# Kernel optimization log

Measured on AMD Instinct MI355X. Metric: run time of the kernel, lower is better.

The kernel has to match this reference:

```python
import jax, jax.numpy as jnp
import numpy as np

# Model dims (match init_kwargs)
E = 2048   # embed_dim
H = 16     # num_heads
QR = 512   # q_low_rank
KVR = 512  # kv_low_rank
DR = 64    # rope_dim
DV = 128   # v_head_dim
S = 2048   # seq_len


def _make_rotary(seq_len, dim):
    inv_freq = 1.0 / jnp.power(10000.0, jnp.arange(0, dim, 2, dtype=jnp.float32) / dim)
    t = jnp.arange(seq_len, dtype=jnp.float32)
    freqs = jnp.outer(t, inv_freq)  # (S, dim//2)
    return jnp.sin(freqs), jnp.cos(freqs)


def _apply_rope(x, sin, cos):
    # x: (S, H_or_1, D); sin/cos: (S, D//2)
    d = x.shape[-1] // 2
    x1, x2 = x[..., :d], x[..., d:]
    s = jnp.concatenate([sin, sin], axis=-1)[:, None, :]
    c = jnp.concatenate([cos, cos], axis=-1)[:, None, :]
    return x * c + jnp.concatenate([-x2, x1], axis=-1) * s


def setup_inputs() -> dict:
    key = jax.random.key(0)
    ks = jax.random.split(key, 8)
    def lin(k, out_dim, in_dim):
        return jax.random.normal(k, (out_dim, in_dim), dtype=jnp.float32) * (1.0 / np.sqrt(in_dim))
    return {
        "x": jax.random.normal(ks[0], (S, E), dtype=jnp.float32),
        "wq_down": lin(ks[1], QR, E),
        "wq_up": lin(ks[2], H * DV, QR),
        "wq_rope": lin(ks[3], H * DR, QR),
        "wkv_down": lin(ks[4], KVR, E),
        "wkv_up": lin(ks[5], H * 2 * DV, KVR),
        "wk_rope": lin(ks[6], DR, E),
        "wo": lin(ks[7], E, H * DV),
    }


def reference(x, wq_down, wq_up, wq_rope, wkv_down, wkv_up, wk_rope, wo):
    seq = x.shape[0]
    # Query path: low-rank bottleneck -> content + rope streams
    c_q = x @ wq_down.T                                   # (S, QR)
    q_content = (c_q @ wq_up.T).reshape(seq, H, DV)       # (S, H, DV)
    q_rope = (c_q @ wq_rope.T).reshape(seq, H, DR)        # (S, H, DR)
    # KV path: shared low-rank bottleneck
    c_kv = x @ wkv_down.T                                 # (S, KVR)
    kv = c_kv @ wkv_up.T                                  # (S, 2*H*DV)
    k_content_flat, v_flat = jnp.split(kv, 2, axis=-1)
    k_content = k_content_flat.reshape(seq, H, DV)
    v = v_flat.reshape(seq, H, DV)
    # Shared key-RoPE projection (one per position, broadcast over heads)
    k_rope_shared = (x @ wk_rope.T)[:, None, :]           # (S, 1, DR)
    sin, cos = _make_rotary(seq, DR)
    q_rope_rot = _apply_rope(q_rope, sin, cos)            # (S, H, DR)
    k_rope_rot = _apply_rope(k_rope_shared, sin, cos)     # (S, 1, DR)
    # Concat content + rope streams; QK head dim = DV + DR
    dt = jnp.bfloat16
    q = jnp.concatenate([q_content, q_rope_rot], axis=-1).astype(dt)                            # (S, H, DV+DR)
    k = jnp.concatenate([k_content, jnp.broadcast_to(k_rope_rot, (seq, H, DR))], axis=-1).astype(dt)
    v_attn = v.astype(dt)
    scale = 1.0 / np.sqrt(DV + DR)
    # Attention. Note: original zero-pads V to DV+DR then slices output back to
    # DV -- mathematically identical to attending with unpadded V.
    logits = jnp.einsum('shd,thd->hst', q, k).astype(jnp.float32) * scale  # (H, S, S)
    probs = jax.nn.softmax(logits, axis=-1).astype(dt)
    attn = jnp.einsum('hst,thd->shd', probs, v_attn)      # (S, H, DV)
    attn_flat = attn.reshape(seq, H * DV)
    return (attn_flat @ wo.T).astype(jnp.float32)         # (S, E)
```

## Files before the change

kernel.cpp:

```cpp
#include <hip/hip_runtime.h>
#include <stdint.h>
#include <math.h>

#define S_LEN 2048
#define NH 16

typedef __attribute__((ext_vector_type(8))) short bf16x8;
typedef __attribute__((ext_vector_type(4))) float f32x4;
typedef __attribute__((ext_vector_type(16))) float f32x16;
typedef unsigned short ush;

__device__ __forceinline__ ush f2bf(float f) {
  union { float f; unsigned u; } v; v.f = f;
  unsigned x = v.u;
  return (ush)((x + 0x7fffu + ((x >> 16) & 1u)) >> 16);
}
__device__ __forceinline__ float bf2f(ush b) {
  union { unsigned u; float f; } v; v.u = ((unsigned)b) << 16;
  return v.f;
}
__device__ __forceinline__ ush f2h(float f) {
  _Float16 h = (_Float16)f;
  union { _Float16 h; ush u; } v; v.h = h;
  return v.u;
}
__device__ __forceinline__ float h2f(ush u) {
  union { ush u; _Float16 h; } v; v.u = u;
  return (float)v.h;
}
__device__ __forceinline__ uint2 sx32(uint2 v) {
  uint2 r;
  r.x = (unsigned)__shfl_xor((int)v.x, 32, 64);
  r.y = (unsigned)__shfl_xor((int)v.y, 32, 64);
  return r;
}

__device__ __forceinline__ void gload_lds16(const ush* g, ush* l) {
  __builtin_amdgcn_global_load_lds((const __attribute__((address_space(1))) void*)g,
                                   (__attribute__((address_space(3))) void*)l, 16, 0, 0);
}

__global__ void mega_pack(const float* __restrict__ wq_down, const float* __restrict__ wkv_down,
                          const float* __restrict__ wk_rope, const float* __restrict__ wq_up,
                          const float* __restrict__ wq_rope, const float* __restrict__ wkv_up,
                          const float* __restrict__ wo, const float* __restrict__ x,
                          ush* __restrict__ wdh, ush* __restrict__ wqh, ush* __restrict__ wkvuh,
                          ush* __restrict__ woh, ush* __restrict__ xh, float* __restrict__ tab) {
  int idx = blockIdx.x * 256 + threadIdx.x;
  if (idx < 2359296) {
    int r = idx >> 11, c = idx & 2047;
    float v = (r < 512) ? wq_down[(size_t)r * 2048 + c]
            : (r < 1024) ? wkv_down[(size_t)(r - 512) * 2048 + c]
            : (r < 1088) ? wk_rope[(size_t)(r - 1024) * 2048 + c] : 0.f;
    wdh[idx] = f2h(v);
    return;
  }
  idx -= 2359296;
  if (idx < 1572864) {
    int r = idx >> 9, c = idx & 511;
    float v = (r < 2048) ? wq_up[(size_t)r * 512 + c] : wq_rope[(size_t)(r - 2048) * 512 + c];
    wqh[idx] = f2h(v);
    return;
  }
  idx -= 1572864;
  if (idx < 2097152) { wkvuh[idx] = f2h(wkv_up[idx]); return; }
  idx -= 2097152;
  if (idx < 4194304) { woh[idx] = f2h(wo[idx]); return; }
  idx -= 4194304;
  if (idx < 4194304) { xh[idx] = f2h(x[idx]); return; }
  idx -= 4194304;
  if (idx < 65536) {
    int tt = idx >> 5, i = idx & 31;
    float inv_freq = 1.0f / powf(10000.0f, (float)i * (1.0f / 32.0f));
    float fr = (float)tt * inv_freq;
    tab[idx] = sinf(fr);
    tab[65536 + idx] = cosf(fr);
  }
}

__global__ __launch_bounds__(256) void gemm_down(
    const ush* __restrict__ A, const ush* __restrict__ B,
    ush* __restrict__ cqh, ush* __restrict__ ckvh, float* __restrict__ krl) {
  constexpr int K = 2048;
  __shared__ __align__(16) ush As[64 * 32];
  __shared__ __align__(16) ush Bs[64 * 32];
  const int t = threadIdx.x, l = t & 63, w = t >> 6;
  const int wm = w & 1, wn = w >> 1;
  const int m0 = blockIdx.y * 64, n0 = blockIdx.x * 64;
  const int lm = l & 15, lq = l >> 4;
  const int lr = l >> 2, lc = (l & 3) * 8;

  f32x4 acc[2][2];
  const f32x4 zero = {0.f, 0.f, 0.f, 0.f};
#pragma unroll
  for (int i = 0; i < 2; i++)
#pragma unroll
    for (int j = 0; j < 2; j++) acc[i][j] = zero;

  const ush* Ag = A + (size_t)(m0 + w * 16 + lr) * K + lc;
  const ush* Bg = B + (size_t)(n0 + w * 16 + lr) * K + lc;
  ush* Al = As + w * 512;
  ush* Bl = Bs + w * 512;

  for (int k0 = 0; k0 < K; k0 += 32) {
    __syncthreads();
    gload_lds16(Ag + k0, Al);
    gload_lds16(Bg + k0, Bl);
    __syncthreads();
    bf16x8 af[2], bfr[2];
#pragma unroll
    for (int i = 0; i < 2; i++)
      af[i] = *(const bf16x8*)(As + (wm * 32 + i * 16 + lm) * 32 + lq * 8);
#pragma unroll
    for (int j = 0; j < 2; j++)
      bfr[j] = *(const bf16x8*)(Bs + (wn * 32 + j * 16 + lm) * 32 + lq * 8);
#pragma unroll
    for (int i = 0; i < 2; i++)
#pragma unroll
      for (int j = 0; j < 2; j++)
        acc[i][j] = __builtin_amdgcn_mfma_f32_16x16x32_f16(af[i], bfr[j], acc[i][j], 0, 0, 0);
  }

#pragma unroll
  for (int i = 0; i < 2; i++)
#pragma unroll
    for (int j = 0; j < 2; j++)
#pragma unroll
      for (int r = 0; r < 4; r++) {
        int mm = m0 + wm * 32 + i * 16 + lq * 4 + r;
        int nn = n0 + wn * 32 + j * 16 + lm;
        float v = acc[i][j][r];
        if (nn < 512)       cqh[(size_t)mm * 512 + nn] = f2h(v);
        else if (nn < 1024) ckvh[(size_t)mm * 512 + nn - 512] = f2h(v);
        else if (nn < 1088) krl[(size_t)mm * 64 + nn - 1024] = v;
      }
}

__global__ __launch_bounds__(256) void gemm_up(
    const ush* __restrict__ cqh, const ush* __restrict__ wqh,
    const ush* __restrict__ ckvh, const ush* __restrict__ wkvuh,
    ush* __restrict__ qupf, ush* __restrict__ kvf) {
  constexpr int BM = 128, BN = 64, K = 512, FI = 4, FJ = 2;
  __shared__ __align__(16) ush As[BM * 32];
  __shared__ __align__(16) ush Bs[BN * 32];
  int bx = blockIdx.x;
  const ush* A; const ush* B; ush* C; int ldc;
  if (bx < 48) { A = cqh; B = wqh; C = qupf; ldc = 3072; }
  else { bx -= 48; A = ckvh; B = wkvuh; C = kvf; ldc = 4096; }
  const int t = threadIdx.x, l = t & 63, w = t >> 6;
  const int wm = w & 1, wn = w >> 1;
  const int m0 = blockIdx.y * BM, n0 = bx * BN;
  const int lm = l & 15, lq = l >> 4;
  const int lr = l >> 2, lc = (l & 3) * 8;

  f32x4 acc[FI][FJ];
  const f32x4 zero = {0.f, 0.f, 0.f, 0.f};
#pragma unroll
  for (int i = 0; i < FI; i++)
#pragma unroll
    for (int j = 0; j < FJ; j++) acc[i][j] = zero;

  const ush* Ag[2];
#pragma unroll
  for (int i = 0; i < 2; i++) Ag[i] = A + (size_t)(m0 + w * 32 + i * 16 + lr) * K + lc;
  const ush* Bg = B + (size_t)(n0 + w * 16 + lr) * K + lc;
  ush* Al = As + w * (BM * 8);
  ush* Bl = Bs + w * (BN * 8);

  for (int k0 = 0; k0 < K; k0 += 32) {
    __syncthreads();
#pragma unroll
    for (int i = 0; i < 2; i++) gload_lds16(Ag[i] + k0, Al + i * 512);
    gload_lds16(Bg + k0, Bl);
    __syncthreads();
    bf16x8 af[FI], bfr[FJ];
#pragma unroll
    for (int i = 0; i < FI; i++)
      af[i] = *(const bf16x8*)(As + (wm * 64 + i * 16 + lm) * 32 + lq * 8);
#pragma unroll
    for (int j = 0; j < FJ; j++)
      bfr[j] = *(const bf16x8*)(Bs + (wn * 32 + j * 16 + lm) * 32 + lq * 8);
#pragma unroll
    for (int i = 0; i < FI; i++)
#pragma unroll
      for (int j = 0; j < FJ; j++)
        acc[i][j] = __builtin_amdgcn_mfma_f32_16x16x32_f16(af[i], bfr[j], acc[i][j], 0, 0, 0);
  }

#pragma unroll
  for (int i = 0; i < FI; i++)
#pragma unroll
    for (int j = 0; j < FJ; j++)
#pragma unroll
      for (int r = 0; r < 4; r++) {
        int mm = m0 + wm * 64 + i * 16 + lq * 4 + r;
        int nn = n0 + wn * 32 + j * 16 + lm;
        C[(size_t)mm * ldc + nn] = f2h(acc[i][j][r]);
      }
}

__global__ __launch_bounds__(256) void gemm_out(
    const ush* __restrict__ A, const ush* __restrict__ B, float* __restrict__ C,
    int K, int ldc) {
  constexpr int BM = 128, BN = 64, FI = 4, FJ = 2;
  __shared__ __align__(16) ush As[BM * 32];
  __shared__ __align__(16) ush Bs[BN * 32];
  const int t = threadIdx.x, l = t & 63, w = t >> 6;
  const int wm = w & 1, wn = w >> 1;
  const int m0 = blockIdx.y * BM, n0 = blockIdx.x * BN;
  const int lm = l & 15, lq = l >> 4;
  const int lr = l >> 2, lc = (l & 3) * 8;

  f32x4 acc[FI][FJ];
  const f32x4 zero = {0.f, 0.f, 0.f, 0.f};
#pragma unroll
  for (int i = 0; i < FI; i++)
#pragma unroll
    for (int j = 0; j < FJ; j++) acc[i][j] = zero;

  const ush* Ag[2];
#pragma unroll
  for (int i = 0; i < 2; i++) Ag[i] = A + (size_t)(m0 + w * 32 + i * 16 + lr) * K + lc;
  const ush* Bg = B + (size_t)(n0 + w * 16 + lr) * K + lc;
  ush* Al = As + w * (BM * 8);
  ush* Bl = Bs + w * (BN * 8);

  for (int k0 = 0; k0 < K; k0 += 32) {
    __syncthreads();
#pragma unroll
    for (int i = 0; i < 2; i++) gload_lds16(Ag[i] + k0, Al + i * 512);
    gload_lds16(Bg + k0, Bl);
    __syncthreads();
    bf16x8 af[FI], bfr[FJ];
#pragma unroll
    for (int i = 0; i < FI; i++)
      af[i] = *(const bf16x8*)(As + (wm * 64 + i * 16 + lm) * 32 + lq * 8);
#pragma unroll
    for (int j = 0; j < FJ; j++)
      bfr[j] = *(const bf16x8*)(Bs + (wn * 32 + j * 16 + lm) * 32 + lq * 8);
#pragma unroll
    for (int i = 0; i < FI; i++)
#pragma unroll
      for (int j = 0; j < FJ; j++)
        acc[i][j] = __builtin_amdgcn_mfma_f32_16x16x32_f16(af[i], bfr[j], acc[i][j], 0, 0, 0);
  }

#pragma unroll
  for (int i = 0; i < FI; i++)
#pragma unroll
    for (int j = 0; j < FJ; j++)
#pragma unroll
      for (int r = 0; r < 4; r++) {
        int mm = m0 + wm * 64 + i * 16 + lq * 4 + r;
        int nn = n0 + wn * 32 + j * 16 + lm;
        C[(size_t)mm * ldc + nn] = acc[i][j][r];
      }
}

__global__ void build_all(const ush* __restrict__ qupf, const ush* __restrict__ kvf,
                          const float* __restrict__ krl, const float* __restrict__ tab,
                          ush* __restrict__ qb, ush* __restrict__ kbt, ush* __restrict__ vtt) {
  const float scale = 0.07216878364870323f;
  if (blockIdx.x >= 50176) {
    __shared__ ush Vt[128 * 72];
    int b = blockIdx.x - 50176;
    const int T = b & 31, h = b >> 5, t = threadIdx.x;
    const int key = t >> 5, d0 = (t & 31) * 4;
#pragma unroll
    for (int pass = 0; pass < 8; ++pass) {
      int k = key + pass * 8;
      int s = T * 64 + k;
      ushort4 v = *(const ushort4*)(kvf + (size_t)s * 4096 + 2048 + h * 128 + d0);
      Vt[(d0 + 0) * 72 + k] = f2bf(h2f(v.x));
      Vt[(d0 + 1) * 72 + k] = f2bf(h2f(v.y));
      Vt[(d0 + 2) * 72 + k] = f2bf(h2f(v.z));
      Vt[(d0 + 3) * 72 + k] = f2bf(h2f(v.w));
    }
    __syncthreads();
    ush* dst = vtt + (size_t)(h * 32 + T) * 9216;
    for (int off = t; off < 1152; off += 256) {
      int row = off / 9, c8 = (off % 9) * 8;
      *(bf16x8*)(dst + row * 72 + c8) = *(const bf16x8*)(Vt + row * 72 + c8);
    }
    return;
  }
  int idx = blockIdx.x * 256 + threadIdx.x;
  if (idx < 6291456) {
    int d = idx % 192; int sh = idx / 192; int h = sh & 15; int s = sh >> 4;
    ush v;
    if (d < 128) {
      v = f2bf(h2f(qupf[(size_t)s * 3072 + h * 128 + d]) * scale);
    } else {
      int r = d - 128, i = r & 31;
      float sn = tab[s * 32 + i], cs = tab[65536 + s * 32 + i];
      const ush* qr = qupf + (size_t)s * 3072 + 2048 + h * 64;
      float xv = h2f(qr[r]);
      float other = (r < 32) ? -h2f(qr[r + 32]) : h2f(qr[r - 32]);
      v = f2bf((xv * cs + other * sn) * scale);
    }
    qb[((size_t)h * S_LEN + s) * 192 + d] = v;
    return;
  }
  idx -= 6291456;
  if (idx < 6553600) {
    int c = idx % 200; int r2 = idx / 200;
    int key = r2 & 63; int r3 = r2 >> 6; int T = r3 & 31; int h = r3 >> 5;
    int s = T * 64 + key;
    ush v = 0;
    if (c < 128) {
      v = f2bf(h2f(kvf[(size_t)s * 4096 + h * 128 + c]));
    } else if (c < 192) {
      int r = c - 128, i = r & 31;
      float sn = tab[s * 32 + i], cs = tab[65536 + s * 32 + i];
      const float* kr = krl + (size_t)s * 64;
      float xv = kr[r];
      float other = (r < 32) ? -kr[r + 32] : kr[r - 32];
      v = f2bf(xv * cs + other * sn);
    }
    kbt[((size_t)(h * 32 + T) * 64 + key) * 200 + c] = v;
  }
}

__global__ __launch_bounds__(256) void attn_fused(
    const ush* __restrict__ qb, const ush* __restrict__ kbt, const ush* __restrict__ vtt,
    ush* __restrict__ opart, float* __restrict__ ml) {
  __shared__ __align__(16) ush Ks[64 * 200];
  __shared__ __align__(16) ush Vs[128 * 72];
  const int t = threadIdx.x, l = t & 63, w = t >> 6;
  const int h = blockIdx.y, z = blockIdx.z;
  const int qrow0 = blockIdx.x * 128 + w * 32;
  const int ln = l & 31, lh = l >> 5;

  bf16x8 qf[12];
#pragma unroll
  for (int st = 0; st < 12; st++)
    qf[st] = *(const bf16x8*)(qb + ((size_t)h * S_LEN + qrow0 + ln) * 192 + st * 16 + lh * 8);

  f32x16 o[4];
#pragma unroll
  for (int i = 0; i < 4; i++)
#pragma unroll
    for (int r = 0; r < 16; r++) o[i][r] = 0.f;
  float ps = 0.f;

  for (int it = 0; it < 8; ++it) {
    const int T = z * 8 + it;
    const ush* ksrc = kbt + (size_t)(h * 32 + T) * 12800;
    const ush* vsrc = vtt + (size_t)(h * 32 + T) * 9216;
    __syncthreads();
    for (int i = w; i < 25; i += 4) gload_lds16(ksrc + i * 512 + l * 8, Ks + i * 512);
    for (int i = w; i < 18; i += 4) gload_lds16(vsrc + i * 512 + l * 8, Vs + i * 512);
    __syncthreads();

    f32x16 sv[2];
#pragma unroll
    for (int kb = 0; kb < 2; kb++)
#pragma unroll
      for (int r = 0; r < 16; r++) sv[kb][r] = 0.f;
#pragma unroll
    for (int kb = 0; kb < 2; kb++)
#pragma unroll
      for (int st = 0; st < 12; st++) {
        bf16x8 af = *(const bf16x8*)(Ks + (kb * 32 + ln) * 200 + st * 16 + lh * 8);
        sv[kb] = __builtin_amdgcn_mfma_f32_32x32x16_bf16(af, qf[st], sv[kb], 0, 0, 0);
      }

#pragma unroll
    for (int kb = 0; kb < 2; kb++) {
      uint2 pk[4];
#pragma unroll
      for (int g = 0; g < 4; g++) {
        float p0 = __expf(sv[kb][4 * g + 0]);
        float p1 = __expf(sv[kb][4 * g + 1]);
        float p2 = __expf(sv[kb][4 * g + 2]);
        float p3 = __expf(sv[kb][4 * g + 3]);
        ps += (p0 + p1) + (p2 + p3);
        union { ush u[4]; uint2 v; } c;
        c.u[0] = f2bf(p0); c.u[1] = f2bf(p1); c.u[2] = f2bf(p2); c.u[3] = f2bf(p3);
        pk[g] = c.v;
      }
      uint2 pg0 = sx32(pk[0]), pg1 = sx32(pk[1]), pg2 = sx32(pk[2]), pg3 = sx32(pk[3]);
      uint2 a0 = lh ? pg1 : pk[0];
      uint2 b0 = lh ? pk[1] : pg0;
      uint2 a1 = lh ? pg3 : pk[2];
      uint2 b1 = lh ? pk[3] : pg2;
      union { unsigned d[4]; bf16x8 v; } pf0u, pf1u;
      pf0u.d[0] = a0.x; pf0u.d[1] = a0.y; pf0u.d[2] = b0.x; pf0u.d[3] = b0.y;
      pf1u.d[0] = a1.x; pf1u.d[1] = a1.y; pf1u.d[2] = b1.x; pf1u.d[3] = b1.y;
#pragma unroll
      for (int db = 0; db < 4; db++) {
        bf16x8 vf0 = *(const bf16x8*)(Vs + (db * 32 + ln) * 72 + kb * 32 + lh * 8);
        bf16x8 vf1 = *(const bf16x8*)(Vs + (db * 32 + ln) * 72 + kb * 32 + 16 + lh * 8);
        o[db] = __builtin_amdgcn_mfma_f32_32x32x16_bf16(vf0, pf0u.v, o[db], 0, 0, 0);
        o[db] = __builtin_amdgcn_mfma_f32_32x32x16_bf16(vf1, pf1u.v, o[db], 0, 0, 0);
      }
    }
  }

  float lsum = ps + __shfl_xor(ps, 32, 64);
  const int s = qrow0 + ln;
  const size_t rbase = ((size_t)((z * 16 + h) * 2048) + s) * 128;
#pragma unroll
  for (int db = 0; db < 4; db++)
#pragma unroll
    for (int rq = 0; rq < 4; rq++) {
      ushort4 v4;
      v4.x = f2h(o[db][rq * 4 + 0] * 0.0625f);
      v4.y = f2h(o[db][rq * 4 + 1] * 0.0625f);
      v4.z = f2h(o[db][rq * 4 + 2] * 0.0625f);
      v4.w = f2h(o[db][rq * 4 + 3] * 0.0625f);
      *(ushort4*)(&opart[rbase + db * 32 + 8 * rq + 4 * lh]) = v4;
    }
  if (lh == 0) ml[(size_t)(z * 16 + h) * 2048 + s] = lsum;
}

__global__ __launch_bounds__(256) void attn_reduce(const ush* __restrict__ opart,
                                                   const float* __restrict__ ml,
                                                   ush* __restrict__ attnh) {
  int row = blockIdx.x * 4 + (threadIdx.x >> 6);
  int l = threadIdx.x & 63;
  int h = row >> 11, s = row & 2047;
  float lsum = 0.f;
#pragma unroll
  for (int z = 0; z < 4; z++) lsum += ml[(size_t)(z * 16 + h) * 2048 + s];
  float inv = 16.0f / lsum;
#pragma unroll
  for (int c0 = 0; c0 < 128; c0 += 64) {
    int c = c0 + l;
    float acc = 0.f;
#pragma unroll
    for (int z = 0; z < 4; z++)
      acc += h2f(opart[((size_t)(z * 16 + h) * 2048 + s) * 128 + c]);
    attnh[(size_t)s * 2048 + h * 128 + c] = f2h(bf2f(f2bf(acc * inv)));
  }
}

extern "C" void kernel_launch(void* const* d_in, const int* in_sizes, int n_in,
                              void* d_out, int out_size, void* d_ws, size_t ws_size,
                              hipStream_t stream) {
  const float* x        = (const float*)d_in[0];
  const float* wq_down  = (const float*)d_in[1];
  const float* wq_up    = (const float*)d_in[2];
  const float* wq_rope  = (const float*)d_in[3];
  const float* wkv_down = (const float*)d_in[4];
  const float* wkv_up   = (const float*)d_in[5];
  const float* wk_rope  = (const float*)d_in[6];
  const float* wo       = (const float*)d_in[7];
  char* ws = (char*)d_ws;

  size_t off = 0;
  auto alloc = [&](size_t b) { size_t c = off; off += (b + 255) & ~(size_t)255; return c; };
  const size_t XH    = alloc(2048UL * 2048 * 2);
  const size_t WDH   = alloc(1152UL * 2048 * 2);
  const size_t KRL   = alloc(2048UL * 64 * 4);
  const size_t CQH   = alloc(2048UL * 512 * 2);
  const size_t CKVH  = alloc(2048UL * 512 * 2);
  const size_t WQH   = alloc(3072UL * 512 * 2);
  const size_t QUPF  = alloc(2048UL * 3072 * 2);
  const size_t WKVUH = alloc(4096UL * 512 * 2);
  const size_t WOH   = alloc(2048UL * 2048 * 2);
  const size_t KVF   = alloc(2048UL * 4096 * 2);
  const size_t QB    = alloc(16UL * 2048 * 192 * 2);
  const size_t KBT   = alloc(16UL * 32 * 12800 * 2);
  const size_t VTT   = alloc(16UL * 32 * 9216 * 2);
  const size_t TAB   = alloc(2048UL * 32 * 4 * 2);
  const size_t OPART = alloc(4UL * 16 * 2048 * 128 * 2);
  const size_t ML    = alloc(4UL * 16 * 2048 * 4);
  const size_t ATTNH = XH;

  mega_pack<<<dim3(56576), 256, 0, stream>>>(
      wq_down, wkv_down, wk_rope, wq_up, wq_rope, wkv_up, wo, x,
      (ush*)(ws + WDH), (ush*)(ws + WQH), (ush*)(ws + WKVUH),
      (ush*)(ws + WOH), (ush*)(ws + XH), (float*)(ws + TAB));

  gemm_down<<<dim3(18, 32), 256, 0, stream>>>(
      (ush*)(ws + XH), (ush*)(ws + WDH),
      (ush*)(ws + CQH), (ush*)(ws + CKVH), (float*)(ws + KRL));

  gemm_up<<<dim3(112, 16), 256, 0, stream>>>(
      (ush*)(ws + CQH), (ush*)(ws + WQH),
      (ush*)(ws + CKVH), (ush*)(ws + WKVUH),
      (ush*)(ws + QUPF), (ush*)(ws + KVF));

  build_all<<<dim3(50688), 256, 0, stream>>>(
      (const ush*)(ws + QUPF), (const ush*)(ws + KVF), (const float*)(ws + KRL),
      (const float*)(ws + TAB), (ush*)(ws + QB), (ush*)(ws + KBT), (ush*)(ws + VTT));

  attn_fused<<<dim3(16, 16, 4), 256, 0, stream>>>(
      (ush*)(ws + QB), (ush*)(ws + KBT), (ush*)(ws + VTT),
      (ush*)(ws + OPART), (float*)(ws + ML));
  attn_reduce<<<dim3(8192), 256, 0, stream>>>((const ush*)(ws + OPART), (const float*)(ws + ML),
                                              (ush*)(ws + ATTNH));

  gemm_out<<<dim3(32, 16), 256, 0, stream>>>(
      (ush*)(ws + ATTNH), (ush*)(ws + WOH), (float*)d_out, 2048, 2048);
}
```

Before: 325.9 us.

## Double-buffer K/V tiles in attention with 512-thread blocks and fewer KV splits

Rebuilds the attention kernel around 8-wave blocks of 256 query rows. K/V tiles are double-buffered in LDS, with the next tile's async global-to-LDS load issued before computing the current one, and explicit waitcnt and barriers. The KV split count drops from 4 to 2, which halves the partial outputs the reduce kernel reads. Block IDs are remapped for scheduling, MFMA sections get raised priority, and the bf16 pack and cross-half shuffle use v_cvt_pk_bf16_f32 and v_permlane32_swap. In exchange the kernel uses twice the LDS and launches fewer blocks, which risks lower occupancy.

```diff
diff --git a/kernel.cpp b/kernel.cpp
--- a/kernel.cpp
+++ b/kernel.cpp
@@ -27,12 +27,6 @@
 __device__ __forceinline__ float h2f(ush u) {
   union { ush u; _Float16 h; } v; v.u = u;
   return (float)v.h;
-}
-__device__ __forceinline__ uint2 sx32(uint2 v) {
-  uint2 r;
-  r.x = (unsigned)__shfl_xor((int)v.x, 32, 64);
-  r.y = (unsigned)__shfl_xor((int)v.y, 32, 64);
-  return r;
 }
 
 __device__ __forceinline__ void gload_lds16(const ush* g, ush* l) {
@@ -321,20 +315,24 @@
   }
 }
 
-__global__ __launch_bounds__(256) void attn_fused(
+__global__ __launch_bounds__(512, 2) void attn_fused(
     const ush* __restrict__ qb, const ush* __restrict__ kbt, const ush* __restrict__ vtt,
     ush* __restrict__ opart, float* __restrict__ ml) {
-  __shared__ __align__(16) ush Ks[64 * 200];
-  __shared__ __align__(16) ush Vs[128 * 72];
+  __shared__ __align__(16) ush Ks[2][64 * 200];
+  __shared__ __align__(16) ush Vs[2][128 * 72];
   const int t = threadIdx.x, l = t & 63, w = t >> 6;
-  const int h = blockIdx.y, z = blockIdx.z;
-  const int qrow0 = blockIdx.x * 128 + w * 32;
+  const int id = blockIdx.x + 8 * (blockIdx.y + 16 * blockIdx.z);
+  const int wid = (id & 7) * 32 + (id >> 3);
+  const int qx = wid & 7, h = (wid >> 3) & 15, z = wid >> 7;
+  const int qrow0 = qx * 256 + w * 32;
   const int ln = l & 31, lh = l >> 5;
 
   bf16x8 qf[12];
 #pragma unroll
   for (int st = 0; st < 12; st++)
     qf[st] = *(const bf16x8*)(qb + ((size_t)h * S_LEN + qrow0 + ln) * 192 + st * 16 + lh * 8);
+#pragma unroll
+  for (int st = 0; st < 12; st++) asm volatile("" : "+v"(qf[st]));
 
   f32x16 o[4];
 #pragma unroll
@@ -343,31 +341,58 @@
     for (int r = 0; r < 16; r++) o[i][r] = 0.f;
   float ps = 0.f;
 
-  for (int it = 0; it < 8; ++it) {
-    const int T = z * 8 + it;
-    const ush* ksrc = kbt + (size_t)(h * 32 + T) * 12800;
-    const ush* vsrc = vtt + (size_t)(h * 32 + T) * 9216;
-    __syncthreads();
-    for (int i = w; i < 25; i += 4) gload_lds16(ksrc + i * 512 + l * 8, Ks + i * 512);
-    for (int i = w; i < 18; i += 4) gload_lds16(vsrc + i * 512 + l * 8, Vs + i * 512);
-    __syncthreads();
+  const ush* kbase = kbt + (size_t)(h * 32 + z * 16) * 12800;
+  const ush* vbase = vtt + (size_t)(h * 32 + z * 16) * 9216;
+
+  for (int c = w; c < 43; c += 8) {
+    if (c < 25) gload_lds16(kbase + c * 512 + l * 8, &Ks[0][c * 512]);
+    else        gload_lds16(vbase + (c - 25) * 512 + l * 8, &Vs[0][(c - 25) * 512]);
+  }
+  asm volatile("s_waitcnt vmcnt(0)" ::: "memory");
+  __builtin_amdgcn_s_barrier();
+  __builtin_amdgcn_sched_barrier(0);
+
+  int cur = 0;
+  for (int it = 0; it < 16; ++it) {
+    if (it < 15) {
+      const ush* ksrc = kbase + (size_t)(it + 1) * 12800;
+      const ush* vsrc = vbase + (size_t)(it + 1) * 9216;
+      ush* kd = &Ks[cur ^ 1][0];
+      ush* vd = &Vs[cur ^ 1][0];
+      for (int c = w; c < 43; c += 8) {
+        if (c < 25) gload_lds16(ksrc + c * 512 + l * 8, kd + c * 512);
+        else        gload_lds16(vsrc + (c - 25) * 512 + l * 8, vd + (c - 25) * 512);
+      }
+      __builtin_amdgcn_sched_barrier(0);
+      asm volatile("s_waitcnt vmcnt(5)" ::: "memory");
+    } else {
+      asm volatile("s_waitcnt vmcnt(0)" ::: "memory");
+    }
+    __builtin_amdgcn_s_barrier();
+    __builtin_amdgcn_sched_barrier(0);
+
+    const ush* Kb = &Ks[cur][0];
+    const ush* Vb = &Vs[cur][0];
 
     f32x16 sv[2];
 #pragma unroll
     for (int kb = 0; kb < 2; kb++)
 #pragma unroll
       for (int r = 0; r < 16; r++) sv[kb][r] = 0.f;
+
+    __builtin_amdgcn_s_setprio(1);
 #pragma unroll
     for (int kb = 0; kb < 2; kb++)
 #pragma unroll
       for (int st = 0; st < 12; st++) {
-        bf16x8 af = *(const bf16x8*)(Ks + (kb * 32 + ln) * 200 + st * 16 + lh * 8);
+        bf16x8 af = *(const bf16x8*)(Kb + (kb * 32 + ln) * 200 + st * 16 + lh * 8);
         sv[kb] = __builtin_amdgcn_mfma_f32_32x32x16_bf16(af, qf[st], sv[kb], 0, 0, 0);
       }
+    __builtin_amdgcn_s_setprio(0);
 
 #pragma unroll
     for (int kb = 0; kb < 2; kb++) {
-      uint2 pk[4];
+      unsigned pk8[8];
 #pragma unroll
       for (int g = 0; g < 4; g++) {
         float p0 = __expf(sv[kb][4 * g + 0]);
@@ -375,26 +400,33 @@
         float p2 = __expf(sv[kb][4 * g + 2]);
         float p3 = __expf(sv[kb][4 * g + 3]);
         ps += (p0 + p1) + (p2 + p3);
-        union { ush u[4]; uint2 v; } c;
-        c.u[0] = f2bf(p0); c.u[1] = f2bf(p1); c.u[2] = f2bf(p2); c.u[3] = f2bf(p3);
-        pk[g] = c.v;
-      }
-      uint2 pg0 = sx32(pk[0]), pg1 = sx32(pk[1]), pg2 = sx32(pk[2]), pg3 = sx32(pk[3]);
-      uint2 a0 = lh ? pg1 : pk[0];
-      uint2 b0 = lh ? pk[1] : pg0;
-      uint2 a1 = lh ? pg3 : pk[2];
-      uint2 b1 = lh ? pk[3] : pg2;
+        unsigned lo, hi;
+        asm("v_cvt_pk_bf16_f32 %0, %1, %2" : "=v"(lo) : "v"(p0), "v"(p1));
+        asm("v_cvt_pk_bf16_f32 %0, %1, %2" : "=v"(hi) : "v"(p2), "v"(p3));
+        pk8[2 * g] = lo; pk8[2 * g + 1] = hi;
+      }
+      asm("v_permlane32_swap_b32 %0, %1" : "+v"(pk8[0]), "+v"(pk8[2]));
+      asm("v_permlane32_swap_b32 %0, %1" : "+v"(pk8[1]), "+v"(pk8[3]));
+      asm("v_permlane32_swap_b32 %0, %1" : "+v"(pk8[4]), "+v"(pk8[6]));
+      asm("v_permlane32_swap_b32 %0, %1" : "+v"(pk8[5]), "+v"(pk8[7]));
       union { unsigned d[4]; bf16x8 v; } pf0u, pf1u;
-      pf0u.d[0] = a0.x; pf0u.d[1] = a0.y; pf0u.d[2] = b0.x; pf0u.d[3] = b0.y;
-      pf1u.d[0] = a1.x; pf1u.d[1] = a1.y; pf1u.d[2] = b1.x; pf1u.d[3] = b1.y;
+      pf0u.d[0] = pk8[0]; pf0u.d[1] = pk8[1]; pf0u.d[2] = pk8[2]; pf0u.d[3] = pk8[3];
+      pf1u.d[0] = pk8[4]; pf1u.d[1] = pk8[5]; pf1u.d[2] = pk8[6]; pf1u.d[3] = pk8[7];
+
+      __builtin_amdgcn_s_setprio(1);
 #pragma unroll
       for (int db = 0; db < 4; db++) {
-        bf16x8 vf0 = *(const bf16x8*)(Vs + (db * 32 + ln) * 72 + kb * 32 + lh * 8);
-        bf16x8 vf1 = *(const bf16x8*)(Vs + (db * 32 + ln) * 72 + kb * 32 + 16 + lh * 8);
+        bf16x8 vf0 = *(const bf16x8*)(Vb + (db * 32 + ln) * 72 + kb * 32 + lh * 8);
+        bf16x8 vf1 = *(const bf16x8*)(Vb + (db * 32 + ln) * 72 + kb * 32 + 16 + lh * 8);
         o[db] = __builtin_amdgcn_mfma_f32_32x32x16_bf16(vf0, pf0u.v, o[db], 0, 0, 0);
         o[db] = __builtin_amdgcn_mfma_f32_32x32x16_bf16(vf1, pf1u.v, o[db], 0, 0, 0);
       }
-    }
+      __builtin_amdgcn_s_setprio(0);
+    }
+
+    __builtin_amdgcn_s_barrier();
+    __builtin_amdgcn_sched_barrier(0);
+    cur ^= 1;
   }
 
   float lsum = ps + __shfl_xor(ps, 32, 64);
@@ -422,14 +454,14 @@
   int h = row >> 11, s = row & 2047;
   float lsum = 0.f;
 #pragma unroll
-  for (int z = 0; z < 4; z++) lsum += ml[(size_t)(z * 16 + h) * 2048 + s];
+  for (int z = 0; z < 2; z++) lsum += ml[(size_t)(z * 16 + h) * 2048 + s];
   float inv = 16.0f / lsum;
 #pragma unroll
   for (int c0 = 0; c0 < 128; c0 += 64) {
     int c = c0 + l;
     float acc = 0.f;
 #pragma unroll
-    for (int z = 0; z < 4; z++)
+    for (int z = 0; z < 2; z++)
       acc += h2f(opart[((size_t)(z * 16 + h) * 2048 + s) * 128 + c]);
     attnh[(size_t)s * 2048 + h * 128 + c] = f2h(bf2f(f2bf(acc * inv)));
   }
@@ -464,8 +496,8 @@
   const size_t KBT   = alloc(16UL * 32 * 12800 * 2);
   const size_t VTT   = alloc(16UL * 32 * 9216 * 2);
   const size_t TAB   = alloc(2048UL * 32 * 4 * 2);
-  const size_t OPART = alloc(4UL * 16 * 2048 * 128 * 2);
-  const size_t ML    = alloc(4UL * 16 * 2048 * 4);
+  const size_t OPART = alloc(2UL * 16 * 2048 * 128 * 2);
+  const size_t ML    = alloc(2UL * 16 * 2048 * 4);
   const size_t ATTNH = XH;
 
   mega_pack<<<dim3(56576), 256, 0, stream>>>(
@@ -486,7 +518,7 @@
       (const ush*)(ws + QUPF), (const ush*)(ws + KVF), (const float*)(ws + KRL),
       (const float*)(ws + TAB), (ush*)(ws + QB), (ush*)(ws + KBT), (ush*)(ws + VTT));
 
-  attn_fused<<<dim3(16, 16, 4), 256, 0, stream>>>(
+  attn_fused<<<dim3(8, 16, 2), 512, 0, stream>>>(
       (ush*)(ws + QB), (ush*)(ws + KBT), (ush*)(ws + VTT),
       (ush*)(ws + OPART), (float*)(ws + ML));
   attn_reduce<<<dim3(8192), 256, 0, stream>>>((const ush*)(ws + OPART), (const float*)(ws + ML),
```

After: 311.6 us. -4.4%, faster.
